# Kernel optimization log

Measured on AMD Instinct MI355X. Metric: run time of the kernel, lower is better.

The kernel has to match this reference:

```python
import jax, jax.numpy as jnp
import numpy as np

B, S, D, H, DFF = 4, 2048, 1024, 16, 4096
DK = D // H
EPS = 1e-6


def setup_inputs() -> dict:
    key = jax.random.key(0)
    ks = jax.random.split(key, 20)
    sc = 0.02
    inp = {
        'x': jax.random.normal(ks[0], (B, S, D), jnp.float32),
        'inp_mask': jax.random.randint(ks[1], (B, 1, 1, S), 0, 2, jnp.int32),
        # linear weights stored [in, out]
        'wq_w': jax.random.normal(ks[2], (D, D), jnp.float32) * sc,
        'wq_b': jnp.zeros((D,), jnp.float32),
        'wk_w': jax.random.normal(ks[3], (D, D), jnp.float32) * sc,
        'wk_b': jnp.zeros((D,), jnp.float32),
        'wv_w': jax.random.normal(ks[4], (D, D), jnp.float32) * sc,
        'wv_b': jnp.zeros((D,), jnp.float32),
        'wo_w': jax.random.normal(ks[5], (D, D), jnp.float32) * sc,
        'wo_b': jnp.zeros((D,), jnp.float32),
        'ff_w0': jax.random.normal(ks[6], (D, DFF), jnp.float32) * sc,
        'ff_b0': jnp.zeros((DFF,), jnp.float32),
        'ff_w1': jax.random.normal(ks[7], (DFF, D), jnp.float32) * sc,
        'ff_b1': jnp.zeros((D,), jnp.float32),
        'ln0_a': jnp.ones((D,), jnp.float32),
        'ln0_b': jnp.zeros((D,), jnp.float32),
        'ln1_a': jnp.ones((D,), jnp.float32),
        'ln1_b': jnp.zeros((D,), jnp.float32),
    }
    return inp


def _layernorm(x, alpha, bias):
    # Faithful to source: unbiased std (Bessel), divide by (std + eps)
    mean = jnp.mean(x, axis=-1, keepdims=True)
    std = jnp.std(x, axis=-1, keepdims=True, ddof=1)
    return alpha * (x - mean) / (std + EPS) + bias


def _mha(x, wq_w, wq_b, wk_w, wk_b, wv_w, wv_b, wo_w, wo_b, mask):
    q = (x @ wq_w + wq_b).reshape(B, S, H, DK).transpose(0, 2, 1, 3)  # [B,H,S,DK]
    k = (x @ wk_w + wk_b).reshape(B, S, H, DK).transpose(0, 2, 1, 3)
    v = (x @ wv_w + wv_b).reshape(B, S, H, DK).transpose(0, 2, 1, 3)
    scores = jnp.einsum('bhqd,bhkd->bhqk', q, k) / jnp.sqrt(jnp.float32(DK))
    scores = jnp.where(mask == 0, jnp.float32(-1e9), scores)
    attn = jax.nn.softmax(scores, axis=-1)
    out = jnp.einsum('bhqk,bhkd->bhqd', attn, v)
    out = out.transpose(0, 2, 1, 3).reshape(B, S, D)
    return out @ wo_w + wo_b


def reference(x, inp_mask, wq_w, wq_b, wk_w, wk_b, wv_w, wv_b, wo_w, wo_b,
              ff_w0, ff_b0, ff_w1, ff_b1, ln0_a, ln0_b, ln1_a, ln1_b):
    # Residual 0: pre-norm MHA (dropout = 0)
    h = _layernorm(x, ln0_a, ln0_b)
    x = x + _mha(h, wq_w, wq_b, wk_w, wk_b, wv_w, wv_b, wo_w, wo_b, inp_mask)
    # Residual 1: pre-norm FFN
    h = _layernorm(x, ln1_a, ln1_b)
    h = jax.nn.gelu(h @ ff_w0 + ff_b0, approximate=False) @ ff_w1 + ff_b1
    return x + h
```

## Files before the change

### kernel.cpp

```cpp
#include <hip/hip_runtime.h>
#include <hip/hip_bf16.h>
#include <math.h>

#define Bc 4
#define Sc 2048
#define Dc 1024
#define Hc 16
#define DKc 64
#define DFFc 4096
#define Mc (Bc*Sc)
#define LN_EPS 1e-6f

typedef unsigned short ushort_t;
typedef short bf16x8 __attribute__((ext_vector_type(8)));
typedef float f32x4 __attribute__((ext_vector_type(4)));
typedef float f32x16 __attribute__((ext_vector_type(16)));

typedef __attribute__((address_space(3))) void lds_void_t;
typedef __attribute__((address_space(1))) const void gconst_void_t;

__device__ __forceinline__ void gload_lds16(const void* g, void* l) {
  __builtin_amdgcn_global_load_lds((gconst_void_t*)g, (lds_void_t*)l, 16, 0, 0);
}

__device__ __forceinline__ ushort_t f2bf(float f) {
  union { float f; unsigned int u; } a; a.f = f;
  unsigned int r = a.u + 0x7fffu + ((a.u >> 16) & 1u);
  return (ushort_t)(r >> 16);
}

__device__ __forceinline__ void swapl(unsigned& a, unsigned& b) {
  asm("v_permlane32_swap_b32 %0, %1" : "+v"(a), "+v"(b));
}
__device__ __forceinline__ unsigned cvtpk_bf16(float lo, float hi) {
  unsigned r;
  asm("v_cvt_pk_bf16_f32 %0, %1, %2" : "=v"(r) : "v"(lo), "v"(hi));
  return r;
}

__global__ __launch_bounds__(256) void k_transpose_cvt(
    const float* __restrict__ W, ushort_t* __restrict__ WT, int K, int N) {
  __shared__ float t[32][33];
  const int tx = threadIdx.x & 31, ty = threadIdx.x >> 5;
  const int n0 = blockIdx.x * 32, k0 = blockIdx.y * 32;
#pragma unroll
  for (int i = 0; i < 4; ++i)
    t[ty + i * 8][tx] = W[(size_t)(k0 + ty + i * 8) * N + n0 + tx];
  __syncthreads();
#pragma unroll
  for (int i = 0; i < 4; ++i)
    WT[(size_t)(n0 + ty + i * 8) * K + k0 + tx] = f2bf(t[tx][ty + i * 8]);
}

__global__ __launch_bounds__(256) void k_layernorm(
    const float* __restrict__ x, const float* __restrict__ alpha,
    const float* __restrict__ beta, ushort_t* __restrict__ out) {
  const int row = blockIdx.x;
  const int tid = threadIdx.x;
  const int w = tid >> 6, lane = tid & 63;
  const float4 v = ((const float4*)(x + (size_t)row * Dc))[tid];
  float s = v.x + v.y + v.z + v.w;
#pragma unroll
  for (int m = 32; m >= 1; m >>= 1) s += __shfl_xor(s, m, 64);
  __shared__ float ws[8];
  if (lane == 0) ws[w] = s;
  __syncthreads();
  s = ws[0] + ws[1] + ws[2] + ws[3];
  const float mean = s * (1.0f / Dc);
  const float dx = v.x - mean, dy = v.y - mean, dz = v.z - mean, dw = v.w - mean;
  float ss = dx * dx + dy * dy + dz * dz + dw * dw;
#pragma unroll
  for (int m = 32; m >= 1; m >>= 1) ss += __shfl_xor(ss, m, 64);
  if (lane == 0) ws[4 + w] = ss;
  __syncthreads();
  ss = ws[4] + ws[5] + ws[6] + ws[7];
  const float stdv = sqrtf(ss / (float)(Dc - 1));
  const float inv = 1.0f / (stdv + LN_EPS);
  const float4 a = ((const float4*)alpha)[tid];
  const float4 b = ((const float4*)beta)[tid];
  ushort4 o;
  o.x = f2bf(a.x * dx * inv + b.x);
  o.y = f2bf(a.y * dy * inv + b.y);
  o.z = f2bf(a.z * dz * inv + b.z);
  o.w = f2bf(a.w * dw * inv + b.w);
  *(ushort4*)(out + (size_t)row * Dc + tid * 4) = o;
}

template <int MODE>
__global__ __launch_bounds__(512, 4) void k_gemm8(
    const ushort_t* __restrict__ A, const ushort_t* __restrict__ BT,
    const float* __restrict__ bias, const float* __restrict__ bias2,
    const float* __restrict__ bias3, const float* __restrict__ resid,
    void* __restrict__ Cout, void* __restrict__ Cout2, void* __restrict__ Cout3,
    int N, int K, int nxn) {
  __shared__ __align__(16) ushort_t As[3][256 * 32];
  __shared__ __align__(16) ushort_t Bs[3][128 * 32];
  const int tid = threadIdx.x;
  const int lane = tid & 63;
  const int wid = tid >> 6;
  const int wm = wid >> 1, wn = wid & 1;
  const int lrow = lane & 15, lgrp = lane >> 4;
  const int xcd = blockIdx.x & 7;
  const int idx = blockIdx.x >> 3;
  const int in_ = xcd * nxn + idx % nxn;
  const int im = idx / nxn;
  const int m0 = im << 8, n0 = in_ << 7;

  const f32x4 zero4 = {0.f, 0.f, 0.f, 0.f};
  f32x4 acc[4][4];
#pragma unroll
  for (int i = 0; i < 4; ++i)
#pragma unroll
    for (int j = 0; j < 4; ++j) acc[i][j] = zero4;

  const int ar0 = tid >> 2;
  const int as0 = (tid & 3) ^ ((ar0 >> 1) & 3);
  const int ar1 = ar0 + 128;
  const ushort_t* Ag0 = A + (size_t)(m0 + ar0) * K + as0 * 8;
  const ushort_t* Ag1 = A + (size_t)(m0 + ar1) * K + as0 * 8;
  const ushort_t* Bg0 = BT + (size_t)(n0 + ar0 % 128) * K + as0 * 8;
  char* const a_w = (char*)(&As[0][0]) + wid * 1024;
  char* const b_w = (char*)(&Bs[0][0]) + wid * 1024;

  const int sl = lgrp ^ ((lrow >> 1) & 3);
  const int aoff = (wm * 64 + lrow) * 32 + sl * 8;
  const int boff = (wn * 64 + lrow) * 32 + sl * 8;

  const int nk = K >> 5;
  {
    gload_lds16(Ag0, a_w);
    gload_lds16(Ag1, a_w + 8192);
    gload_lds16(Bg0, b_w);
    gload_lds16(Ag0 + 32, a_w + 16384);
    gload_lds16(Ag1 + 32, a_w + 16384 + 8192);
    gload_lds16(Bg0 + 32, b_w + 8192);
  }
  int cur = 0;
  for (int t = 0; t < nk; ++t) {
    if (t + 1 < nk) { asm volatile("s_waitcnt vmcnt(3)" ::: "memory"); }
    else            { asm volatile("s_waitcnt vmcnt(0)" ::: "memory"); }
    asm volatile("s_barrier" ::: "memory");
    const ushort_t* Ab = &As[cur][0];
    const ushort_t* Bb = &Bs[cur][0];
    bf16x8 af[4], bf[4];
#pragma unroll
    for (int mf = 0; mf < 4; ++mf) af[mf] = *(const bf16x8*)(Ab + aoff + mf * 512);
#pragma unroll
    for (int nf = 0; nf < 4; ++nf) bf[nf] = *(const bf16x8*)(Bb + boff + nf * 512);
    if (t + 2 < nk) {
      const int bi = (cur + 2 >= 3) ? cur - 1 : cur + 2;
      const size_t ko = (size_t)(t + 2) * 32;
      gload_lds16(Ag0 + ko, a_w + bi * 16384);
      gload_lds16(Ag1 + ko, a_w + bi * 16384 + 8192);
      gload_lds16(Bg0 + ko, b_w + bi * 8192);
    }
    __builtin_amdgcn_s_setprio(1);
#pragma unroll
    for (int mf = 0; mf < 4; ++mf)
#pragma unroll
      for (int nf = 0; nf < 4; ++nf)
        acc[mf][nf] = __builtin_amdgcn_mfma_f32_16x16x32_bf16(af[mf], bf[nf], acc[mf][nf], 0, 0, 0);
    __builtin_amdgcn_s_setprio(0);
    asm volatile("s_barrier" ::: "memory");
    cur = (cur + 1 == 3) ? 0 : cur + 1;
  }

  const float* bsrc = bias;
  int n0l = n0;
  int seg = 0;
  if (MODE == 4) {
    seg = n0 >> 10;
    n0l = n0 & 1023;
    bsrc = (seg == 0) ? bias : (seg == 1 ? bias2 : bias3);
  }
  float bv[4];
#pragma unroll
  for (int n = 0; n < 4; ++n) bv[n] = bsrc[n0l + wn * 64 + n * 16 + lrow];

#pragma unroll
  for (int m = 0; m < 4; ++m)
#pragma unroll
    for (int n = 0; n < 4; ++n) {
      if (MODE == 4 && seg == 2) {
        const size_t s0 = (size_t)(m0 + wm * 64 + m * 16 + lgrp * 4);
        const int gb = (int)(s0 >> 11);
        const int ss = (int)(s0 & 2047);
        const int col = n0l + wn * 64 + n * 16 + lrow;
        const int hh = col >> 6, dd = col & 63;
        ushort4 o4;
        o4.x = f2bf(acc[m][n][0] + bv[n]);
        o4.y = f2bf(acc[m][n][1] + bv[n]);
        o4.z = f2bf(acc[m][n][2] + bv[n]);
        o4.w = f2bf(acc[m][n][3] + bv[n]);
        *(ushort4*)((ushort_t*)Cout3 + ((size_t)(gb * Hc + hh) * DKc + dd) * Sc + ss) = o4;
      } else if (MODE == 4) {
        ushort_t* Co = (seg == 0) ? (ushort_t*)Cout : (ushort_t*)Cout2;
        const int col = n0l + wn * 64 + n * 16 + lrow;
#pragma unroll
        for (int r = 0; r < 4; ++r) {
          const size_t row = (size_t)(m0 + wm * 64 + m * 16 + lgrp * 4 + r);
          Co[row * Dc + col] = f2bf(acc[m][n][r] + bv[n]);
        }
      } else {
#pragma unroll
        for (int r = 0; r < 4; ++r) {
          const size_t row = (size_t)(m0 + wm * 64 + m * 16 + lgrp * 4 + r);
          const size_t col = (size_t)(n0 + wn * 64 + n * 16 + lrow);
          float v = acc[m][n][r] + bv[n];
          if (MODE == 2) {
            const float u = 0.7978845608f * (v + 0.044715f * v * v * v);
            const float e = exp2f(2.885390082f * u);
            const float th = 1.0f - 2.0f * __frcp_rn(e + 1.0f);
            v = 0.5f * v * (1.0f + th);
          }
          if (MODE == 1) {
            v += resid[row * N + col];
            ((float*)Cout)[row * N + col] = v;
          } else {
            ((ushort_t*)Cout)[row * N + col] = f2bf(v);
          }
        }
      }
    }
}

__global__ __launch_bounds__(256) void k_maskadd(const int* __restrict__ mask,
                                                float* __restrict__ madd, int n) {
  const int i = blockIdx.x * 256 + threadIdx.x;
  if (i < n) madd[i] = mask[i] ? -8.0f : -1.442695041e9f;
}

#define KSCALE 0.1803368801e0f
__global__ __launch_bounds__(512) void k_attn11(
    const ushort_t* __restrict__ Qb, const ushort_t* __restrict__ Kb,
    const ushort_t* __restrict__ Vt, const float* __restrict__ madd,
    ushort_t* __restrict__ Ob) {
  __shared__ __align__(16) ushort_t Ks[4][32 * 64];
  __shared__ __align__(16) ushort_t Vs[4][64 * 32];
  __shared__ __align__(16) float Ms[Sc];

  const int bid = blockIdx.x;
  const int xcd = bid & 7, idx = bid >> 3;
  const int bh = xcd * 8 + (idx >> 3);
  const int qb = idx & 7;
  const int b = bh >> 4, h = bh & 15;
  const int tid = threadIdx.x;
  const int lane = tid & 63, w = tid >> 6;
  const int l31 = lane & 31, hi = lane >> 5;
  const size_t bS = (size_t)b * Sc;
  const int qrow0 = qb * 256 + w * 32;

  bf16x8 qf[4];
  const ushort_t* qp = Qb + (bS + qrow0 + l31) * Dc + h * DKc + hi * 8;
#pragma unroll
  for (int c = 0; c < 4; ++c) qf[c] = *(const bf16x8*)(qp + c * 16);

  bf16x8 ones;
#pragma unroll
  for (int i = 0; i < 8; ++i) ones[i] = (short)0x3F80;

  f32x16 accA, accB, accS;
#pragma unroll
  for (int i = 0; i < 16; ++i) { accA[i] = 0.f; accB[i] = 0.f; accS[i] = 0.f; }

  const ushort_t* Vth = Vt + (size_t)bh * (DKc * Sc);
  const float* mp = madd + b * Sc;

  const int c0 = tid & 255;
  const int kr = c0 >> 3, ksl = (c0 & 7) ^ (kr & 7);
  const int vr = c0 >> 2, vsl = (c0 & 3) ^ ((vr >> 1) & 3);
  const ushort_t* Kg = Kb + (bS + kr) * Dc + h * DKc + ksl * 8;
  const ushort_t* Vg = Vth + (size_t)vr * Sc + vsl * 8;
  char* const k_w = (char*)(&Ks[0][0]) + (w & 3) * 1024;
  char* const v_w = (char*)(&Vs[0][0]) + (w & 3) * 1024;

  gload_lds16(mp + tid * 4, (char*)Ms + w * 1024);
  if (w < 4) {
    gload_lds16(Kg, k_w);
    gload_lds16(Kg + (size_t)32 * Dc, k_w + 4096);
  } else {
    gload_lds16(Vg, v_w);
    gload_lds16(Vg + 32, v_w + 4096);
  }

  const int vsw = (l31 >> 1) & 3;
  int cur = 0;
  f32x16 scA, scB;

  auto qk_phase = [&](f32x16& scN, int t) {
    const char* Kbuf = (const char*)(&Ks[cur][0]);
    bf16x8 kf[4];
#pragma unroll
    for (int c = 0; c < 4; ++c) {
      const int slr = (c * 2 + hi) ^ (l31 & 7);
      kf[c] = *(const bf16x8*)(Kbuf + l31 * 128 + slr * 16);
    }
    if (t + 2 < 64) {
      const int bi = (cur + 2) & 3;
      const size_t kv2 = (size_t)(t + 2) * 32;
      if (w < 4) gload_lds16(Kg + kv2 * Dc, k_w + bi * 4096);
      else       gload_lds16(Vg + kv2, v_w + bi * 4096);
    }
#pragma unroll
    for (int i = 0; i < 16; ++i) scN[i] = 0.f;
    __builtin_amdgcn_s_setprio(1);
    scN = __builtin_amdgcn_mfma_f32_32x32x16_bf16(kf[0], qf[0], scN, 0, 0, 0);
    scN = __builtin_amdgcn_mfma_f32_32x32x16_bf16(kf[1], qf[1], scN, 0, 0, 0);
    scN = __builtin_amdgcn_mfma_f32_32x32x16_bf16(kf[2], qf[2], scN, 0, 0, 0);
    scN = __builtin_amdgcn_mfma_f32_32x32x16_bf16(kf[3], qf[3], scN, 0, 0, 0);
    __builtin_amdgcn_s_setprio(0);
  };

  auto sm_pv = [&](f32x16& scP, int tp) {
    float4 mv[4];
#pragma unroll
    for (int c = 0; c < 4; ++c)
      mv[c] = *(const float4*)(&Ms[tp * 32 + c * 8 + 4 * hi]);
    const char* Vbuf = (const char*)(&Vs[(cur + 3) & 3][0]);
    const bf16x8 v00 = *(const bf16x8*)(Vbuf + l31 * 64 + ((hi ^ vsw) * 16));
    const bf16x8 v01 = *(const bf16x8*)(Vbuf + l31 * 64 + (((2 + hi) ^ vsw) * 16));
    const bf16x8 v10 = *(const bf16x8*)(Vbuf + (32 + l31) * 64 + ((hi ^ vsw) * 16));
    const bf16x8 v11 = *(const bf16x8*)(Vbuf + (32 + l31) * 64 + (((2 + hi) ^ vsw) * 16));
    float p[16];
    p[0] = exp2f(scP[0] * KSCALE + mv[0].x);  p[1] = exp2f(scP[1] * KSCALE + mv[0].y);
    p[2] = exp2f(scP[2] * KSCALE + mv[0].z);  p[3] = exp2f(scP[3] * KSCALE + mv[0].w);
    p[4] = exp2f(scP[4] * KSCALE + mv[1].x);  p[5] = exp2f(scP[5] * KSCALE + mv[1].y);
    p[6] = exp2f(scP[6] * KSCALE + mv[1].z);  p[7] = exp2f(scP[7] * KSCALE + mv[1].w);
    p[8] = exp2f(scP[8] * KSCALE + mv[2].x);  p[9] = exp2f(scP[9] * KSCALE + mv[2].y);
    p[10] = exp2f(scP[10] * KSCALE + mv[2].z); p[11] = exp2f(scP[11] * KSCALE + mv[2].w);
    p[12] = exp2f(scP[12] * KSCALE + mv[3].x); p[13] = exp2f(scP[13] * KSCALE + mv[3].y);
    p[14] = exp2f(scP[14] * KSCALE + mv[3].z); p[15] = exp2f(scP[15] * KSCALE + mv[3].w);
    unsigned cw[4][2];
#pragma unroll
    for (int a = 0; a < 4; ++a) {
      cw[a][0] = cvtpk_bf16(p[4 * a + 0], p[4 * a + 1]);
      cw[a][1] = cvtpk_bf16(p[4 * a + 2], p[4 * a + 3]);
    }
    unsigned a00 = cw[0][0], b00 = cw[1][0]; swapl(a00, b00);
    unsigned a01 = cw[0][1], b01 = cw[1][1]; swapl(a01, b01);
    unsigned a10 = cw[2][0], b10 = cw[3][0]; swapl(a10, b10);
    unsigned a11 = cw[2][1], b11 = cw[3][1]; swapl(a11, b11);
    union { unsigned u[4]; bf16x8 v; } pa0, pa1;
    pa0.u[0] = a00; pa0.u[1] = a01; pa0.u[2] = b00; pa0.u[3] = b01;
    pa1.u[0] = a10; pa1.u[1] = a11; pa1.u[2] = b10; pa1.u[3] = b11;
    __builtin_amdgcn_s_setprio(1);
    accA = __builtin_amdgcn_mfma_f32_32x32x16_bf16(pa0.v, v00, accA, 0, 0, 0);
    accA = __builtin_amdgcn_mfma_f32_32x32x16_bf16(pa1.v, v01, accA, 0, 0, 0);
    accB = __builtin_amdgcn_mfma_f32_32x32x16_bf16(pa0.v, v10, accB, 0, 0, 0);
    accB = __builtin_amdgcn_mfma_f32_32x32x16_bf16(pa1.v, v11, accB, 0, 0, 0);
    accS = __builtin_amdgcn_mfma_f32_32x32x16_bf16(pa0.v, ones, accS, 0, 0, 0);
    accS = __builtin_amdgcn_mfma_f32_32x32x16_bf16(pa1.v, ones, accS, 0, 0, 0);
    __builtin_amdgcn_s_setprio(0);
  };

  asm volatile("s_waitcnt vmcnt(1)" ::: "memory");
  asm volatile("s_barrier" ::: "memory");
  qk_phase(scA, 0);
  cur = 1;
  for (int t = 1; t < 63; t += 2) {
    asm volatile("s_waitcnt vmcnt(1)" ::: "memory");
    asm volatile("s_barrier" ::: "memory");
    qk_phase(scB, t);
    sm_pv(scA, t - 1);
    cur = (cur + 1) & 3;
    asm volatile("s_waitcnt vmcnt(1)" ::: "memory");
    asm volatile("s_barrier" ::: "memory");
    qk_phase(scA, t + 1);
    sm_pv(scB, t);
    cur = (cur + 1) & 3;
  }
  asm volatile("s_waitcnt vmcnt(0)" ::: "memory");
  asm volatile("s_barrier" ::: "memory");
  qk_phase(scB, 63);
  sm_pv(scA, 62);
  cur = (cur + 1) & 3;
  sm_pv(scB, 63);

#pragma unroll
  for (int r = 0; r < 16; ++r) {
    const int q = (r & 3) + 8 * (r >> 2) + 4 * hi;
    const float inv = 1.0f / accS[r];
    ushort_t* op = Ob + (bS + qrow0 + q) * Dc + h * DKc + l31;
    op[0] = f2bf(accA[r] * inv);
    op[32] = f2bf(accB[r] * inv);
  }
}

extern "C" void kernel_launch(void* const* d_in, const int* in_sizes, int n_in,
                              void* d_out, int out_size, void* d_ws, size_t ws_size,
                              hipStream_t stream) {
  const float* x     = (const float*)d_in[0];
  const int* mask    = (const int*)d_in[1];
  const float* wq_w  = (const float*)d_in[2];
  const float* wq_b  = (const float*)d_in[3];
  const float* wk_w  = (const float*)d_in[4];
  const float* wk_b  = (const float*)d_in[5];
  const float* wv_w  = (const float*)d_in[6];
  const float* wv_b  = (const float*)d_in[7];
  const float* wo_w  = (const float*)d_in[8];
  const float* wo_b  = (const float*)d_in[9];
  const float* ff_w0 = (const float*)d_in[10];
  const float* ff_b0 = (const float*)d_in[11];
  const float* ff_w1 = (const float*)d_in[12];
  const float* ff_b1 = (const float*)d_in[13];
  const float* ln0_a = (const float*)d_in[14];
  const float* ln0_b = (const float*)d_in[15];
  const float* ln1_a = (const float*)d_in[16];
  const float* ln1_b = (const float*)d_in[17];
  float* out = (float*)d_out;

  char* ws = (char*)d_ws;
  size_t off = 0;
  ushort_t* WTq = (ushort_t*)(ws + off); off += (size_t)Dc * Dc * 2;
  ushort_t* WTk = (ushort_t*)(ws + off); off += (size_t)Dc * Dc * 2;
  ushort_t* WTv = (ushort_t*)(ws + off); off += (size_t)Dc * Dc * 2;
  ushort_t* WTo = (ushort_t*)(ws + off); off += (size_t)Dc * Dc * 2;
  ushort_t* WT0 = (ushort_t*)(ws + off); off += (size_t)DFFc * Dc * 2;
  ushort_t* WT1 = (ushort_t*)(ws + off); off += (size_t)Dc * DFFc * 2;
  ushort_t* hbuf = (ushort_t*)(ws + off); off += (size_t)Mc * Dc * 2;
  ushort_t* qbuf = (ushort_t*)(ws + off); off += (size_t)Mc * Dc * 2;
  ushort_t* kbuf = (ushort_t*)(ws + off); off += (size_t)Mc * Dc * 2;
  ushort_t* vtb  = (ushort_t*)(ws + off); off += (size_t)Mc * Dc * 2;
  ushort_t* abuf = (ushort_t*)(ws + off); off += (size_t)Mc * Dc * 2;
  float* maddb   = (float*)(ws + off);   off += (size_t)Bc * Sc * 4;
  ushort_t* gbuf = qbuf;

  const dim3 blk(256);
  const dim3 blk512(512);
  k_transpose_cvt<<<dim3(Dc / 32, Dc / 32), blk, 0, stream>>>(wq_w, WTq, Dc, Dc);
  k_transpose_cvt<<<dim3(Dc / 32, Dc / 32), blk, 0, stream>>>(wk_w, WTk, Dc, Dc);
  k_transpose_cvt<<<dim3(Dc / 32, Dc / 32), blk, 0, stream>>>(wv_w, WTv, Dc, Dc);
  k_transpose_cvt<<<dim3(Dc / 32, Dc / 32), blk, 0, stream>>>(wo_w, WTo, Dc, Dc);
  k_transpose_cvt<<<dim3(DFFc / 32, Dc / 32), blk, 0, stream>>>(ff_w0, WT0, Dc, DFFc);
  k_transpose_cvt<<<dim3(Dc / 32, DFFc / 32), blk, 0, stream>>>(ff_w1, WT1, DFFc, Dc);
  k_maskadd<<<dim3((Bc * Sc + 255) / 256), blk, 0, stream>>>(mask, maddb, Bc * Sc);
  k_layernorm<<<Mc, blk, 0, stream>>>(x, ln0_a, ln0_b, hbuf);
  k_gemm8<4><<<dim3(768), blk512, 0, stream>>>(hbuf, WTq, wq_b, wk_b, wv_b, nullptr,
                                               qbuf, kbuf, vtb, 3072, Dc, 3);
  k_attn11<<<dim3(512), blk512, 0, stream>>>(qbuf, kbuf, vtb, maddb, abuf);
  k_gemm8<1><<<dim3(256), blk512, 0, stream>>>(abuf, WTo, wo_b, nullptr, nullptr, x,
                                               out, nullptr, nullptr, Dc, Dc, 1);
  k_layernorm<<<Mc, blk, 0, stream>>>(out, ln1_a, ln1_b, hbuf);
  k_gemm8<2><<<dim3(1024), blk512, 0, stream>>>(hbuf, WT0, ff_b0, nullptr, nullptr, nullptr,
                                                gbuf, nullptr, nullptr, DFFc, Dc, 4);
  k_gemm8<1><<<dim3(256), blk512, 0, stream>>>(gbuf, WT1, ff_b1, nullptr, nullptr, out,
                                               out, nullptr, nullptr, Dc, DFFc, 1);
}
```

Baseline: 456.5 us.

## Compact unmasked keys and skip fully masked key tiles in attention

A new prefix-scan kernel builds a per-batch compaction index of unmasked key positions, a compacted additive mask and a per-batch tile count. The QKV GEMM scatters K and transposed V rows into compacted positions, so attention loops only over about as many 32-key tiles as there are valid keys instead of all 64. This targets the attention FLOPs and K/V loads spent on keys that contribute zero to the softmax. In exchange, K/V epilogue stores become per-element scattered writes with an index lookup. Padding slots in the last tile read uninitialized K/V workspace, relying on the -1e9 mask to zero them out, and an all-masked batch no longer matches the reference's uniform softmax.

Result: faster. 422.2 us (-7.5%).

```diff
diff --git a/kernel.cpp b/kernel.cpp
--- a/kernel.cpp
+++ b/kernel.cpp
@@ -86,11 +86,55 @@
   *(ushort4*)(out + (size_t)row * Dc + tid * 4) = o;
 }
 
+__global__ __launch_bounds__(256) void k_compact(const int* __restrict__ mask,
+                                                 int* __restrict__ cidx,
+                                                 float* __restrict__ cmadd,
+                                                 int* __restrict__ ntile) {
+  const int b = blockIdx.x;
+  const int tid = threadIdx.x;
+  const int base = b * Sc;
+  for (int i = tid; i < Sc; i += 256) cmadd[base + i] = -1.442695041e9f;
+  int mloc[8];
+  int cnt = 0;
+#pragma unroll
+  for (int j = 0; j < 8; ++j) {
+    mloc[j] = mask[base + tid * 8 + j];
+    cnt += mloc[j];
+  }
+  __shared__ int ps[256];
+  ps[tid] = cnt;
+  __syncthreads();
+  for (int ofs = 1; ofs < 256; ofs <<= 1) {
+    const int v = (tid >= ofs) ? ps[tid - ofs] : 0;
+    __syncthreads();
+    ps[tid] += v;
+    __syncthreads();
+  }
+  const int total = ps[255];
+  int run = tid ? ps[tid - 1] : 0;
+#pragma unroll
+  for (int j = 0; j < 8; ++j) {
+    const int gi = base + tid * 8 + j;
+    if (mloc[j]) {
+      cidx[gi] = run;
+      cmadd[base + run] = -8.0f;
+      run++;
+    } else {
+      cidx[gi] = -1;
+    }
+  }
+  if (tid == 0) {
+    int nt = (total + 31) >> 5;
+    ntile[b] = nt < 1 ? 1 : nt;
+  }
+}
+
 template <int MODE>
 __global__ __launch_bounds__(512, 4) void k_gemm8(
     const ushort_t* __restrict__ A, const ushort_t* __restrict__ BT,
     const float* __restrict__ bias, const float* __restrict__ bias2,
     const float* __restrict__ bias3, const float* __restrict__ resid,
+    const int* __restrict__ cidx,
     void* __restrict__ Cout, void* __restrict__ Cout2, void* __restrict__ Cout3,
     int N, int K, int nxn) {
   __shared__ __align__(16) ushort_t As[3][256 * 32];
@@ -182,24 +226,36 @@
 #pragma unroll
     for (int n = 0; n < 4; ++n) {
       if (MODE == 4 && seg == 2) {
-        const size_t s0 = (size_t)(m0 + wm * 64 + m * 16 + lgrp * 4);
-        const int gb = (int)(s0 >> 11);
-        const int ss = (int)(s0 & 2047);
         const int col = n0l + wn * 64 + n * 16 + lrow;
         const int hh = col >> 6, dd = col & 63;
-        ushort4 o4;
-        o4.x = f2bf(acc[m][n][0] + bv[n]);
-        o4.y = f2bf(acc[m][n][1] + bv[n]);
-        o4.z = f2bf(acc[m][n][2] + bv[n]);
-        o4.w = f2bf(acc[m][n][3] + bv[n]);
-        *(ushort4*)((ushort_t*)Cout3 + ((size_t)(gb * Hc + hh) * DKc + dd) * Sc + ss) = o4;
+#pragma unroll
+        for (int r = 0; r < 4; ++r) {
+          const int grow = m0 + wm * 64 + m * 16 + lgrp * 4 + r;
+          const int cp = cidx[grow];
+          if (cp >= 0) {
+            const int gb = grow >> 11;
+            ((ushort_t*)Cout3)[((size_t)(gb * Hc + hh) * DKc + dd) * Sc + cp] =
+                f2bf(acc[m][n][r] + bv[n]);
+          }
+        }
+      } else if (MODE == 4 && seg == 1) {
+        const int col = n0l + wn * 64 + n * 16 + lrow;
+#pragma unroll
+        for (int r = 0; r < 4; ++r) {
+          const int grow = m0 + wm * 64 + m * 16 + lgrp * 4 + r;
+          const int cp = cidx[grow];
+          if (cp >= 0) {
+            const int gb = grow >> 11;
+            ((ushort_t*)Cout2)[(size_t)(gb * Sc + cp) * Dc + col] =
+                f2bf(acc[m][n][r] + bv[n]);
+          }
+        }
       } else if (MODE == 4) {
-        ushort_t* Co = (seg == 0) ? (ushort_t*)Cout : (ushort_t*)Cout2;
         const int col = n0l + wn * 64 + n * 16 + lrow;
 #pragma unroll
         for (int r = 0; r < 4; ++r) {
           const size_t row = (size_t)(m0 + wm * 64 + m * 16 + lgrp * 4 + r);
-          Co[row * Dc + col] = f2bf(acc[m][n][r] + bv[n]);
+          ((ushort_t*)Cout)[row * Dc + col] = f2bf(acc[m][n][r] + bv[n]);
         }
       } else {
 #pragma unroll
@@ -224,17 +280,11 @@
     }
 }
 
-__global__ __launch_bounds__(256) void k_maskadd(const int* __restrict__ mask,
-                                                float* __restrict__ madd, int n) {
-  const int i = blockIdx.x * 256 + threadIdx.x;
-  if (i < n) madd[i] = mask[i] ? -8.0f : -1.442695041e9f;
-}
-
 #define KSCALE 0.1803368801e0f
-__global__ __launch_bounds__(512) void k_attn11(
+__global__ __launch_bounds__(512) void k_attn12(
     const ushort_t* __restrict__ Qb, const ushort_t* __restrict__ Kb,
     const ushort_t* __restrict__ Vt, const float* __restrict__ madd,
-    ushort_t* __restrict__ Ob) {
+    const int* __restrict__ ntile, ushort_t* __restrict__ Ob) {
   __shared__ __align__(16) ushort_t Ks[4][32 * 64];
   __shared__ __align__(16) ushort_t Vs[4][64 * 32];
   __shared__ __align__(16) float Ms[Sc];
@@ -244,6 +294,7 @@
   const int bh = xcd * 8 + (idx >> 3);
   const int qb = idx & 7;
   const int b = bh >> 4, h = bh & 15;
+  const int nt = ntile[b];
   const int tid = threadIdx.x;
   const int lane = tid & 63, w = tid >> 6;
   const int l31 = lane & 31, hi = lane >> 5;
@@ -357,7 +408,8 @@
   asm volatile("s_barrier" ::: "memory");
   qk_phase(scA, 0);
   cur = 1;
-  for (int t = 1; t < 63; t += 2) {
+  int t = 1;
+  for (; t + 1 < nt; t += 2) {
     asm volatile("s_waitcnt vmcnt(1)" ::: "memory");
     asm volatile("s_barrier" ::: "memory");
     qk_phase(scB, t);
@@ -369,12 +421,18 @@
     sm_pv(scB, t);
     cur = (cur + 1) & 3;
   }
-  asm volatile("s_waitcnt vmcnt(0)" ::: "memory");
-  asm volatile("s_barrier" ::: "memory");
-  qk_phase(scB, 63);
-  sm_pv(scA, 62);
-  cur = (cur + 1) & 3;
-  sm_pv(scB, 63);
+  if (t < nt) {
+    asm volatile("s_waitcnt vmcnt(1)" ::: "memory");
+    asm volatile("s_barrier" ::: "memory");
+    qk_phase(scB, t);
+    sm_pv(scA, t - 1);
+    cur = (cur + 1) & 3;
+    asm volatile("s_waitcnt vmcnt(0)" ::: "memory");
+    sm_pv(scB, t);
+  } else {
+    asm volatile("s_waitcnt vmcnt(0)" ::: "memory");
+    sm_pv(scA, nt - 1);
+  }
 
 #pragma unroll
   for (int r = 0; r < 16; ++r) {
@@ -423,6 +481,8 @@
   ushort_t* vtb  = (ushort_t*)(ws + off); off += (size_t)Mc * Dc * 2;
   ushort_t* abuf = (ushort_t*)(ws + off); off += (size_t)Mc * Dc * 2;
   float* maddb   = (float*)(ws + off);   off += (size_t)Bc * Sc * 4;
+  int* cidxb     = (int*)(ws + off);     off += (size_t)Mc * 4;
+  int* ntileb    = (int*)(ws + off);     off += 64;
   ushort_t* gbuf = qbuf;
 
   const dim3 blk(256);
@@ -433,16 +493,16 @@
   k_transpose_cvt<<<dim3(Dc / 32, Dc / 32), blk, 0, stream>>>(wo_w, WTo, Dc, Dc);
   k_transpose_cvt<<<dim3(DFFc / 32, Dc / 32), blk, 0, stream>>>(ff_w0, WT0, Dc, DFFc);
   k_transpose_cvt<<<dim3(Dc / 32, DFFc / 32), blk, 0, stream>>>(ff_w1, WT1, DFFc, Dc);
-  k_maskadd<<<dim3((Bc * Sc + 255) / 256), blk, 0, stream>>>(mask, maddb, Bc * Sc);
+  k_compact<<<dim3(Bc), blk, 0, stream>>>(mask, cidxb, maddb, ntileb);
   k_layernorm<<<Mc, blk, 0, stream>>>(x, ln0_a, ln0_b, hbuf);
   k_gemm8<4><<<dim3(768), blk512, 0, stream>>>(hbuf, WTq, wq_b, wk_b, wv_b, nullptr,
-                                               qbuf, kbuf, vtb, 3072, Dc, 3);
-  k_attn11<<<dim3(512), blk512, 0, stream>>>(qbuf, kbuf, vtb, maddb, abuf);
+                                               cidxb, qbuf, kbuf, vtb, 3072, Dc, 3);
+  k_attn12<<<dim3(512), blk512, 0, stream>>>(qbuf, kbuf, vtb, maddb, ntileb, abuf);
   k_gemm8<1><<<dim3(256), blk512, 0, stream>>>(abuf, WTo, wo_b, nullptr, nullptr, x,
-                                               out, nullptr, nullptr, Dc, Dc, 1);
+                                               nullptr, out, nullptr, nullptr, Dc, Dc, 1);
   k_layernorm<<<Mc, blk, 0, stream>>>(out, ln1_a, ln1_b, hbuf);
   k_gemm8<2><<<dim3(1024), blk512, 0, stream>>>(hbuf, WT0, ff_b0, nullptr, nullptr, nullptr,
-                                                gbuf, nullptr, nullptr, DFFc, Dc, 4);
+                                                nullptr, gbuf, nullptr, nullptr, DFFc, Dc, 4);
   k_gemm8<1><<<dim3(256), blk512, 0, stream>>>(gbuf, WT1, ff_b1, nullptr, nullptr, out,
-                                               out, nullptr, nullptr, Dc, DFFc, 1);
-}
+                                               nullptr, out, nullptr, nullptr, Dc, DFFc, 1);
+}
```
